# Performance work log

Measured on AMD Instinct MI355X. Metric: run time of the kernel, lower is better.

Reference implementation:

```python
import jax, jax.numpy as jnp
import numpy as np

D_MODEL = 1024
NHEAD = 16
HEAD_DIM = D_MODEL // NHEAD  # 64
Q_STRIDE = 2
KV_STRIDE = 1
ROPE_BASE = 10000.0


def _rope_tables(positions):
    # positions: [L] int -> cos/sin [L, HEAD_DIM]
    half = HEAD_DIM // 2
    inv_freq = 1.0 / (ROPE_BASE ** (jnp.arange(half, dtype=jnp.float32) / half))
    freqs = positions.astype(jnp.float32)[:, None] * inv_freq[None, :]  # [L, half]
    emb = jnp.concatenate([freqs, freqs], axis=-1)  # [L, HEAD_DIM]
    return jnp.cos(emb), jnp.sin(emb)


def _rotate_half(x):
    half = x.shape[-1] // 2
    return jnp.concatenate([-x[..., half:], x[..., :half]], axis=-1)


def _apply_rope(x, cos, sin):
    # x: [B, H, L, D]; cos/sin: [L, D] broadcast over B, H
    return x * cos + _rotate_half(x) * sin


def setup_inputs() -> dict:
    key = jax.random.key(0)
    ks = jax.random.split(key, 10)
    B, S, K = 4, 1024, 2048
    s = 0.02
    return {
        "query": jax.random.normal(ks[0], (B, S, D_MODEL), jnp.float32),
        "kv": jax.random.normal(ks[1], (B, K, D_MODEL), jnp.float32),
        "q_w": jax.random.normal(ks[2], (D_MODEL, D_MODEL), jnp.float32) * s,
        "q_b": jax.random.normal(ks[3], (D_MODEL,), jnp.float32) * s,
        "k_w": jax.random.normal(ks[4], (D_MODEL, D_MODEL), jnp.float32) * s,
        "k_b": jax.random.normal(ks[5], (D_MODEL,), jnp.float32) * s,
        "v_w": jax.random.normal(ks[6], (D_MODEL, D_MODEL), jnp.float32) * s,
        "v_b": jax.random.normal(ks[7], (D_MODEL,), jnp.float32) * s,
        "out_w": jax.random.normal(ks[8], (D_MODEL, D_MODEL), jnp.float32) * s,
        "out_b": jax.random.normal(ks[9], (D_MODEL,), jnp.float32) * s,
    }


def reference(query, kv, q_w, q_b, k_w, k_b, v_w, v_b, out_w, out_b):
    B, S, _ = query.shape
    K = kv.shape[1]
    # Projections (torch Linear: x @ W^T + b), reshape to [B, H, L, D]
    q = (query @ q_w.T + q_b).reshape(B, S, NHEAD, HEAD_DIM).transpose(0, 2, 1, 3)
    k = (kv @ k_w.T + k_b).reshape(B, K, NHEAD, HEAD_DIM).transpose(0, 2, 1, 3)
    v = (kv @ v_w.T + v_b).reshape(B, K, NHEAD, HEAD_DIM).transpose(0, 2, 1, 3)
    # RoPE at strided original frame positions
    q_cos, q_sin = _rope_tables(jnp.arange(S) * Q_STRIDE)
    k_cos, k_sin = _rope_tables(jnp.arange(K) * KV_STRIDE)
    q = _apply_rope(q, q_cos, q_sin)
    k = _apply_rope(k, k_cos, k_sin)
    scale = 1.0 / np.sqrt(HEAD_DIM).astype(np.float32)
    attn = jnp.einsum('bhsd,bhkd->bhsk', q, k) * scale  # [B, H, S, K]
    attn = jax.nn.softmax(attn, axis=-1)
    out = jnp.einsum('bhsk,bhkd->bhsd', attn, v)
    out = out.transpose(0, 2, 1, 3).reshape(B, S, D_MODEL)
    return out @ out_w.T + out_b
```

## Files before the change

kernel.cpp:

```cpp
#include <hip/hip_runtime.h>
#include <hip/hip_bf16.h>

#define D_MODEL 1024
#define NHEAD   16
#define HD      64
#define SQ      1024
#define SK      2048

typedef __attribute__((ext_vector_type(8))) short bh8;
typedef __attribute__((ext_vector_type(4))) float fx4;

#define QSCALE 0.1803368801111204f

__device__ __forceinline__ unsigned short f2bf(float f) {
  union { float f; unsigned u; } v; v.f = f;
  return (unsigned short)((v.u + 0x7FFFu + ((v.u >> 16) & 1u)) >> 16);
}

__device__ __forceinline__ float bf2f(unsigned short u) {
  union { unsigned u; float f; } v; v.u = ((unsigned)u) << 16; return v.f;
}

#define GLOAD_LDS16(gp, lp)                                                  \
  __builtin_amdgcn_global_load_lds(                                         \
      (const __attribute__((address_space(1))) unsigned int*)(gp),          \
      (__attribute__((address_space(3))) unsigned int*)(lp), 16, 0, 0)

__global__ __launch_bounds__(256) void cvt_kernel(
    const float* __restrict__ q, const float* __restrict__ kv,
    const float* __restrict__ qw, const float* __restrict__ kw,
    const float* __restrict__ vw, const float* __restrict__ ow,
    unsigned short* __restrict__ qx, unsigned short* __restrict__ kvx,
    unsigned short* __restrict__ qwx, unsigned short* __restrict__ kwx,
    unsigned short* __restrict__ vwx, unsigned short* __restrict__ owx)
{
  const int idx = blockIdx.x * 256 + threadIdx.x;
  const float* src; unsigned short* dst; size_t off;
  if (idx < 524288)        { src = q;  dst = qx;  off = idx; }
  else if (idx < 1572864)  { src = kv; dst = kvx; off = idx - 524288; }
  else {
    const int w = idx - 1572864; const int sel = w >> 17; off = w & 131071;
    src = sel == 0 ? qw : sel == 1 ? kw : sel == 2 ? vw : ow;
    dst = sel == 0 ? qwx : sel == 1 ? kwx : sel == 2 ? vwx : owx;
  }
  const float4 a = ((const float4*)src)[off * 2];
  const float4 b = ((const float4*)src)[off * 2 + 1];
  bh8 r;
  r[0] = (short)f2bf(a.x); r[1] = (short)f2bf(a.y);
  r[2] = (short)f2bf(a.z); r[3] = (short)f2bf(a.w);
  r[4] = (short)f2bf(b.x); r[5] = (short)f2bf(b.y);
  r[6] = (short)f2bf(b.z); r[7] = (short)f2bf(b.w);
  *(bh8*)(dst + off * 8) = r;
}

__global__ __launch_bounds__(256) void qkv_kernel(
    const unsigned short* __restrict__ qx, const unsigned short* __restrict__ kvx,
    const unsigned short* __restrict__ qw, const unsigned short* __restrict__ kw,
    const unsigned short* __restrict__ vw,
    const float* __restrict__ qb, const float* __restrict__ kb,
    const float* __restrict__ vb,
    unsigned short* __restrict__ outq, unsigned short* __restrict__ outk,
    unsigned short* __restrict__ outv)
{
  __shared__ unsigned short Alds[4096];
  __shared__ unsigned short Blds[8192];

  const int t = threadIdx.x;
  const int lane = t & 63, w = t >> 6;
  const int lr = lane & 15, g = lane >> 4;
  const int bid = blockIdx.x;
  const bool isQ = bid >= 2048;
  int bx, by;
  if (isQ) {
    const int tq = bid - 2048;
    const int nq = (tq & 7) * 64 + (tq >> 3);
    bx = nq & 7; by = nq >> 3;
  } else {
    const int nk = (bid & 7) * 256 + (bid >> 3);
    bx = nk & 15; by = nk >> 4;
  }
  const int row0 = by * 64;
  const int colB = bx * 128;
  const int wrow = (w >> 1) * 32;
  const int wcol = (w & 1) * 64;

  const unsigned short* X = isQ ? qx : kvx;
  const unsigned short* Wsrc; const float* bias; int colW; bool isK = false;
  if (isQ)              { Wsrc = qw; bias = qb; colW = colB; }
  else if (colB < 1024) { Wsrc = kw; bias = kb; colW = colB; isK = true; }
  else                  { Wsrc = vw; bias = vb; colW = colB - 1024; }

  const int rbase = t >> 3;
  const int sw8 = (((t & 7) ^ (rbase & 7))) * 8;
  const int sl0 = ((g) ^ (lr & 7)) * 8;
  const int sl1 = ((4 + g) ^ (lr & 7)) * 8;

  fx4 acc[2][4] = {};
  for (int k0 = 0; k0 < 1024; k0 += 64) {
    __syncthreads();
#pragma unroll
    for (int l = 0; l < 2; ++l)
      GLOAD_LDS16(X + (size_t)(row0 + rbase + l * 32) * 1024 + k0 + sw8,
                  &Alds[l * 2048 + t * 8]);
#pragma unroll
    for (int l = 0; l < 4; ++l)
      GLOAD_LDS16(Wsrc + (size_t)(colW + rbase + l * 32) * 1024 + k0 + sw8,
                  &Blds[l * 2048 + t * 8]);
    __syncthreads();

#pragma unroll
    for (int kk = 0; kk < 2; ++kk) {
      const int sl = kk ? sl1 : sl0;
      bh8 af[2], bf[4];
#pragma unroll
      for (int mi = 0; mi < 2; ++mi)
        af[mi] = *(const bh8*)&Alds[(wrow + mi * 16 + lr) * 64 + sl];
#pragma unroll
      for (int ni = 0; ni < 4; ++ni)
        bf[ni] = *(const bh8*)&Blds[(wcol + ni * 16 + lr) * 64 + sl];
      __builtin_amdgcn_s_setprio(1);
#pragma unroll
      for (int mi = 0; mi < 2; ++mi)
#pragma unroll
        for (int ni = 0; ni < 4; ++ni)
          acc[mi][ni] = __builtin_amdgcn_mfma_f32_16x16x32_bf16(af[mi], bf[ni], acc[mi][ni], 0, 0, 0);
      __builtin_amdgcn_s_setprio(0);
    }
  }

  float bv[4];
#pragma unroll
  for (int ni = 0; ni < 4; ++ni) bv[ni] = bias[colW + wcol + ni * 16 + lr];
#pragma unroll
  for (int mi = 0; mi < 2; ++mi)
#pragma unroll
    for (int ni = 0; ni < 4; ++ni)
#pragma unroll
      for (int j = 0; j < 4; ++j) acc[mi][ni][j] += bv[ni];

  const int LMASK = isQ ? 1023 : 2047;
  if (isQ || isK) {
    const float c0 = 0.41524101186092029f;
    const float invf0 = exp2f(-(float)lr * c0);
    const float invf1 = exp2f(-(float)(16 + lr) * c0);
#pragma unroll
    for (int mi = 0; mi < 2; ++mi)
#pragma unroll
      for (int j = 0; j < 4; ++j) {
        const int rg = row0 + wrow + mi * 16 + 4 * g + j;
        const int s = rg & LMASK;
        const float pos = (float)(isQ ? 2 * s : s);
#pragma unroll
        for (int ni = 0; ni < 2; ++ni) {
          float sn, cs;
          __sincosf(pos * (ni == 0 ? invf0 : invf1), &sn, &cs);
          const float x1 = acc[mi][ni][j], x2 = acc[mi][ni + 2][j];
          acc[mi][ni][j]     = x1 * cs - x2 * sn;
          acc[mi][ni + 2][j] = x2 * cs + x1 * sn;
        }
      }
  }

  const int h = (colW + wcol) >> 6;
#pragma unroll
  for (int mi = 0; mi < 2; ++mi)
#pragma unroll
    for (int j = 0; j < 4; ++j) {
      const int rg = row0 + wrow + mi * 16 + 4 * g + j;
      const int bb = isQ ? (rg >> 10) : (rg >> 11);
      const int s = rg & LMASK;
#pragma unroll
      for (int ni = 0; ni < 4; ++ni) {
        const int d = ni * 16 + lr;
        if (isQ) {
          outq[(((size_t)(bb * 16 + h)) * SQ + s) * 64 + d] = f2bf(acc[mi][ni][j] * QSCALE);
        } else {
          const size_t base = ((size_t)(bb * 16 + h)) * (SK * 64);
          if (isK)
            outk[base + (s >> 4) * 1024 + (d >> 5) * 512 + ((d >> 3) & 3) * 128 + (s & 15) * 8 + (d & 7)]
                = f2bf(acc[mi][ni][j]);
          else
            outv[base + (s >> 5) * 2048 + (d >> 4) * 512 + ((s >> 3) & 3) * 128 + (d & 15) * 8 + (s & 7)]
                = f2bf(acc[mi][ni][j]);
        }
      }
    }
}

__global__ __launch_bounds__(256) void oproj_kernel(
    const unsigned short* __restrict__ A, const unsigned short* __restrict__ W,
    const float* __restrict__ bias, float* __restrict__ out)
{
  __shared__ unsigned short Alds[4096];
  __shared__ unsigned short Blds[8192];

  const int t = threadIdx.x;
  const int lane = t & 63, w = t >> 6;
  const int lr = lane & 15, g = lane >> 4;
  const int bid = blockIdx.x;
  const int nb = (bid & 7) * 64 + (bid >> 3);
  const int bx = nb & 7, by = nb >> 3;
  const int row0 = by * 64;
  const int colB = bx * 128;
  const int wrow = (w >> 1) * 32;
  const int wcol = (w & 1) * 64;

  const int rbase = t >> 3;
  const int sw8 = (((t & 7) ^ (rbase & 7))) * 8;
  const int sl0 = ((g) ^ (lr & 7)) * 8;
  const int sl1 = ((4 + g) ^ (lr & 7)) * 8;

  fx4 acc[2][4] = {};
  for (int k0 = 0; k0 < 1024; k0 += 64) {
    __syncthreads();
#pragma unroll
    for (int l = 0; l < 2; ++l)
      GLOAD_LDS16(A + (size_t)(row0 + rbase + l * 32) * 1024 + k0 + sw8,
                  &Alds[l * 2048 + t * 8]);
#pragma unroll
    for (int l = 0; l < 4; ++l)
      GLOAD_LDS16(W + (size_t)(colB + rbase + l * 32) * 1024 + k0 + sw8,
                  &Blds[l * 2048 + t * 8]);
    __syncthreads();

#pragma unroll
    for (int kk = 0; kk < 2; ++kk) {
      const int sl = kk ? sl1 : sl0;
      bh8 af[2], bf[4];
#pragma unroll
      for (int mi = 0; mi < 2; ++mi)
        af[mi] = *(const bh8*)&Alds[(wrow + mi * 16 + lr) * 64 + sl];
#pragma unroll
      for (int ni = 0; ni < 4; ++ni)
        bf[ni] = *(const bh8*)&Blds[(wcol + ni * 16 + lr) * 64 + sl];
      __builtin_amdgcn_s_setprio(1);
#pragma unroll
      for (int mi = 0; mi < 2; ++mi)
#pragma unroll
        for (int ni = 0; ni < 4; ++ni)
          acc[mi][ni] = __builtin_amdgcn_mfma_f32_16x16x32_bf16(af[mi], bf[ni], acc[mi][ni], 0, 0, 0);
      __builtin_amdgcn_s_setprio(0);
    }
  }

  float bv[4];
#pragma unroll
  for (int ni = 0; ni < 4; ++ni) bv[ni] = bias[colB + wcol + ni * 16 + lr];
#pragma unroll
  for (int mi = 0; mi < 2; ++mi)
#pragma unroll
    for (int j = 0; j < 4; ++j) {
      const int rg = row0 + wrow + mi * 16 + 4 * g + j;
#pragma unroll
      for (int ni = 0; ni < 4; ++ni)
        out[(size_t)rg * 1024 + colB + wcol + ni * 16 + lr] = acc[mi][ni][j] + bv[ni];
    }
}

__global__ __launch_bounds__(256, 4) void attn_kernel(
    const unsigned short* __restrict__ Qr, const unsigned short* __restrict__ Kt,
    const unsigned short* __restrict__ Vt, unsigned short* __restrict__ O)
{
  __shared__ __align__(16) unsigned short smem[4 * 2304];
  __shared__ float llds[4][32];

  const int lane = threadIdx.x & 63;
  const int w = threadIdx.x >> 6;
  const int lr = lane & 15, g = lane >> 4, kl = g * 8;
  const int bid = blockIdx.x;
  const int swz = (bid & 7) * 256 + (bid >> 3);
  const int bh = swz >> 5;
  const int q0 = (swz & 31) * 32;
  const int b = bh >> 4, h = bh & 15;

  unsigned short* p_lds = smem + w * 2304;

  const unsigned short* Qp = Qr + (size_t)bh * SQ * HD;
  const unsigned short* Kp = Kt + (size_t)bh * SK * HD;
  const unsigned short* Vp = Vt + (size_t)bh * SK * HD;

  bh8 qf[2][2];
#pragma unroll
  for (int mi = 0; mi < 2; ++mi)
#pragma unroll
    for (int kk = 0; kk < 2; ++kk)
      qf[mi][kk] = *(const bh8*)(Qp + (size_t)(q0 + mi * 16 + lr) * 64 + kk * 32 + kl);

  bh8 ones;
#pragma unroll
  for (int i = 0; i < 8; ++i) ones[i] = (short)0x3F80;

  fx4 oacc[2][4] = {};
  fx4 lacc[2] = {};

  for (int t = 0; t < 8; ++t) {
    fx4 sacc[2][4] = {};
#pragma unroll
    for (int kk = 0; kk < 2; ++kk) {
      bh8 kf[4];
#pragma unroll
      for (int ni = 0; ni < 4; ++ni)
        kf[ni] = *(const bh8*)(Kp + (size_t)(w * 32 + t * 4 + ni) * 1024 + kk * 512 + g * 128 + lr * 8);
      __builtin_amdgcn_s_setprio(1);
#pragma unroll
      for (int mi = 0; mi < 2; ++mi)
#pragma unroll
        for (int ni = 0; ni < 4; ++ni)
          sacc[mi][ni] = __builtin_amdgcn_mfma_f32_16x16x32_bf16(qf[mi][kk], kf[ni], sacc[mi][ni], 0, 0, 0);
      __builtin_amdgcn_s_setprio(0);
    }

    asm volatile("s_waitcnt lgkmcnt(0)" ::: "memory");
    __builtin_amdgcn_sched_barrier(0);

#pragma unroll
    for (int mi = 0; mi < 2; ++mi)
#pragma unroll
      for (int ni = 0; ni < 4; ++ni) {
        float p0, p1, p2, p3;
        asm("v_exp_f32 %0, %1" : "=v"(p0) : "v"(sacc[mi][ni][0]));
        asm("v_exp_f32 %0, %1" : "=v"(p1) : "v"(sacc[mi][ni][1]));
        asm("v_exp_f32 %0, %1" : "=v"(p2) : "v"(sacc[mi][ni][2]));
        asm("v_exp_f32 %0, %1" : "=v"(p3) : "v"(sacc[mi][ni][3]));
        unsigned lo, hi;
        asm("v_cvt_pk_bf16_f32 %0, %1, %2" : "=v"(lo) : "v"(p0), "v"(p1));
        asm("v_cvt_pk_bf16_f32 %0, %1, %2" : "=v"(hi) : "v"(p2), "v"(p3));
        unsigned short* base = &p_lds[(mi * 16 + 4 * g) * 68 + ni * 16 + lr];
        base[0]   = (unsigned short)lo;
        base[68]  = (unsigned short)(lo >> 16);
        base[136] = (unsigned short)hi;
        base[204] = (unsigned short)(hi >> 16);
      }

    asm volatile("s_waitcnt lgkmcnt(0)" ::: "memory");
    __builtin_amdgcn_sched_barrier(0);

#pragma unroll
    for (int kk = 0; kk < 2; ++kk) {
      bh8 pa[2], vb[4];
#pragma unroll
      for (int mi = 0; mi < 2; ++mi) {
        const unsigned short* pp = &p_lds[(mi * 16 + lr) * 68 + kk * 32 + kl];
        const short4 a = *(const short4*)pp;
        const short4 c = *(const short4*)(pp + 4);
        pa[mi][0] = a.x; pa[mi][1] = a.y; pa[mi][2] = a.z; pa[mi][3] = a.w;
        pa[mi][4] = c.x; pa[mi][5] = c.y; pa[mi][6] = c.z; pa[mi][7] = c.w;
      }
#pragma unroll
      for (int ni = 0; ni < 4; ++ni)
        vb[ni] = *(const bh8*)(Vp + (size_t)(w * 16 + t * 2 + kk) * 2048 + ni * 512 + g * 128 + lr * 8);
      __builtin_amdgcn_s_setprio(1);
#pragma unroll
      for (int mi = 0; mi < 2; ++mi) {
#pragma unroll
        for (int ni = 0; ni < 4; ++ni)
          oacc[mi][ni] = __builtin_amdgcn_mfma_f32_16x16x32_bf16(pa[mi], vb[ni], oacc[mi][ni], 0, 0, 0);
        lacc[mi] = __builtin_amdgcn_mfma_f32_16x16x32_bf16(pa[mi], ones, lacc[mi], 0, 0, 0);
      }
      __builtin_amdgcn_s_setprio(0);
    }
  }

  if (lr == 0) {
#pragma unroll
    for (int mi = 0; mi < 2; ++mi)
#pragma unroll
      for (int j = 0; j < 4; ++j)
        llds[w][mi * 16 + 4 * g + j] = lacc[mi][j];
  }

  asm volatile("s_waitcnt lgkmcnt(0)" ::: "memory");
  __builtin_amdgcn_sched_barrier(0);
  unsigned short* opart = smem + w * 2304;
#pragma unroll
  for (int mi = 0; mi < 2; ++mi)
#pragma unroll
    for (int j = 0; j < 4; ++j) {
      const int row = mi * 16 + 4 * g + j;
#pragma unroll
      for (int ni = 0; ni < 4; ++ni)
        opart[row * 72 + ni * 16 + lr] = f2bf(oacc[mi][ni][j]);
    }
  __syncthreads();

  const int row = threadIdx.x >> 3;
  const int d0 = (threadIdx.x & 7) * 8;
  float a8[8] = {};
#pragma unroll
  for (int ww = 0; ww < 4; ++ww) {
    const bh8 v = *(const bh8*)(smem + ww * 2304 + row * 72 + d0);
#pragma unroll
    for (int i = 0; i < 8; ++i) a8[i] += bf2f((unsigned short)v[i]);
  }
  const float inv = 1.0f / (llds[0][row] + llds[1][row] + llds[2][row] + llds[3][row]);
  bh8 r;
#pragma unroll
  for (int i = 0; i < 8; ++i) r[i] = (short)f2bf(a8[i] * inv);
  *(bh8*)&O[((size_t)(b * SQ + q0 + row)) * D_MODEL + h * 64 + d0] = r;
}

extern "C" void kernel_launch(void* const* d_in, const int* in_sizes, int n_in,
                              void* d_out, int out_size, void* d_ws, size_t ws_size,
                              hipStream_t stream) {
  (void)in_sizes; (void)n_in; (void)out_size; (void)ws_size;
  const float* query = (const float*)d_in[0];
  const float* kv    = (const float*)d_in[1];
  const float* q_w   = (const float*)d_in[2];
  const float* q_b   = (const float*)d_in[3];
  const float* k_w   = (const float*)d_in[4];
  const float* k_b   = (const float*)d_in[5];
  const float* v_w   = (const float*)d_in[6];
  const float* v_b   = (const float*)d_in[7];
  const float* out_w = (const float*)d_in[8];
  const float* out_b = (const float*)d_in[9];
  float* out = (float*)d_out;

  unsigned short* ws = (unsigned short*)d_ws;
  unsigned short* qx     = ws;
  unsigned short* kvx    = ws + ((size_t)4  << 20);
  unsigned short* qwx    = ws + ((size_t)12 << 20);
  unsigned short* kwx    = ws + ((size_t)13 << 20);
  unsigned short* vwx    = ws + ((size_t)14 << 20);
  unsigned short* owx    = ws + ((size_t)15 << 20);
  unsigned short* q_rope = ws + ((size_t)16 << 20);
  unsigned short* k_t    = ws + ((size_t)20 << 20);
  unsigned short* v_t    = ws + ((size_t)28 << 20);
  unsigned short* attn_o = qx;

  hipLaunchKernelGGL(cvt_kernel, dim3(8192), dim3(256), 0, stream,
                     query, kv, q_w, k_w, v_w, out_w, qx, kvx, qwx, kwx, vwx, owx);
  hipLaunchKernelGGL(qkv_kernel, dim3(2560), dim3(256), 0, stream,
                     qx, kvx, qwx, kwx, vwx, q_b, k_b, v_b, q_rope, k_t, v_t);
  hipLaunchKernelGGL(attn_kernel, dim3(2048), dim3(256), 0, stream,
                     q_rope, k_t, v_t, attn_o);
  hipLaunchKernelGGL(oproj_kernel, dim3(512), dim3(256), 0, stream,
                     attn_o, owx, out_b, out);
}
```

Baseline: 143.6 us.

## Double-buffer LDS tiles in QKV and output projection GEMMs

Both projection GEMM kernels now keep two LDS buffers for the A and B tiles. Each iteration issues the asynchronous global-to-LDS loads for the next K slice before running MFMAs on the current slice, and needs one barrier per step instead of two. The aim is to hide global load latency behind matrix compute. In exchange, LDS use per block doubles to 48 KB, which may reduce how many blocks fit on each CU.

```diff
diff --git a/kernel.cpp b/kernel.cpp
--- a/kernel.cpp
+++ b/kernel.cpp
@@ -62,8 +62,8 @@
     unsigned short* __restrict__ outq, unsigned short* __restrict__ outk,
     unsigned short* __restrict__ outv)
 {
-  __shared__ unsigned short Alds[4096];
-  __shared__ unsigned short Blds[8192];
+  __shared__ unsigned short Alds[2][4096];
+  __shared__ unsigned short Blds[2][8192];
 
   const int t = threadIdx.x;
   const int lane = t & 63, w = t >> 6;
@@ -95,18 +95,23 @@
   const int sl0 = ((g) ^ (lr & 7)) * 8;
   const int sl1 = ((4 + g) ^ (lr & 7)) * 8;
 
+#define STAGE_P(k0_, bi_) do {                                                        \
+    _Pragma("unroll")                                                                 \
+    for (int l = 0; l < 2; ++l)                                                       \
+      GLOAD_LDS16(X + (size_t)(row0 + rbase + l * 32) * 1024 + (k0_) + sw8,           \
+                  &Alds[bi_][l * 2048 + t * 8]);                                      \
+    _Pragma("unroll")                                                                 \
+    for (int l = 0; l < 4; ++l)                                                       \
+      GLOAD_LDS16(Wsrc + (size_t)(colW + rbase + l * 32) * 1024 + (k0_) + sw8,        \
+                  &Blds[bi_][l * 2048 + t * 8]);                                      \
+  } while (0)
+
   fx4 acc[2][4] = {};
-  for (int k0 = 0; k0 < 1024; k0 += 64) {
+  STAGE_P(0, 0);
+  for (int kt = 0; kt < 16; ++kt) {
+    const int cur = kt & 1;
     __syncthreads();
-#pragma unroll
-    for (int l = 0; l < 2; ++l)
-      GLOAD_LDS16(X + (size_t)(row0 + rbase + l * 32) * 1024 + k0 + sw8,
-                  &Alds[l * 2048 + t * 8]);
-#pragma unroll
-    for (int l = 0; l < 4; ++l)
-      GLOAD_LDS16(Wsrc + (size_t)(colW + rbase + l * 32) * 1024 + k0 + sw8,
-                  &Blds[l * 2048 + t * 8]);
-    __syncthreads();
+    if (kt < 15) STAGE_P((kt + 1) * 64, cur ^ 1);
 
 #pragma unroll
     for (int kk = 0; kk < 2; ++kk) {
@@ -114,10 +119,10 @@
       bh8 af[2], bf[4];
 #pragma unroll
       for (int mi = 0; mi < 2; ++mi)
-        af[mi] = *(const bh8*)&Alds[(wrow + mi * 16 + lr) * 64 + sl];
-#pragma unroll
-      for (int ni = 0; ni < 4; ++ni)
-        bf[ni] = *(const bh8*)&Blds[(wcol + ni * 16 + lr) * 64 + sl];
+        af[mi] = *(const bh8*)&Alds[cur][(wrow + mi * 16 + lr) * 64 + sl];
+#pragma unroll
+      for (int ni = 0; ni < 4; ++ni)
+        bf[ni] = *(const bh8*)&Blds[cur][(wcol + ni * 16 + lr) * 64 + sl];
       __builtin_amdgcn_s_setprio(1);
 #pragma unroll
       for (int mi = 0; mi < 2; ++mi)
@@ -191,8 +196,8 @@
     const unsigned short* __restrict__ A, const unsigned short* __restrict__ W,
     const float* __restrict__ bias, float* __restrict__ out)
 {
-  __shared__ unsigned short Alds[4096];
-  __shared__ unsigned short Blds[8192];
+  __shared__ unsigned short Alds[2][4096];
+  __shared__ unsigned short Blds[2][8192];
 
   const int t = threadIdx.x;
   const int lane = t & 63, w = t >> 6;
@@ -210,18 +215,23 @@
   const int sl0 = ((g) ^ (lr & 7)) * 8;
   const int sl1 = ((4 + g) ^ (lr & 7)) * 8;
 
+#define STAGE_O(k0_, bi_) do {                                                        \
+    _Pragma("unroll")                                                                 \
+    for (int l = 0; l < 2; ++l)                                                       \
+      GLOAD_LDS16(A + (size_t)(row0 + rbase + l * 32) * 1024 + (k0_) + sw8,           \
+                  &Alds[bi_][l * 2048 + t * 8]);                                      \
+    _Pragma("unroll")                                                                 \
+    for (int l = 0; l < 4; ++l)                                                       \
+      GLOAD_LDS16(W + (size_t)(colB + rbase + l * 32) * 1024 + (k0_) + sw8,           \
+                  &Blds[bi_][l * 2048 + t * 8]);                                      \
+  } while (0)
+
   fx4 acc[2][4] = {};
-  for (int k0 = 0; k0 < 1024; k0 += 64) {
+  STAGE_O(0, 0);
+  for (int kt = 0; kt < 16; ++kt) {
+    const int cur = kt & 1;
     __syncthreads();
-#pragma unroll
-    for (int l = 0; l < 2; ++l)
-      GLOAD_LDS16(A + (size_t)(row0 + rbase + l * 32) * 1024 + k0 + sw8,
-                  &Alds[l * 2048 + t * 8]);
-#pragma unroll
-    for (int l = 0; l < 4; ++l)
-      GLOAD_LDS16(W + (size_t)(colB + rbase + l * 32) * 1024 + k0 + sw8,
-                  &Blds[l * 2048 + t * 8]);
-    __syncthreads();
+    if (kt < 15) STAGE_O((kt + 1) * 64, cur ^ 1);
 
 #pragma unroll
     for (int kk = 0; kk < 2; ++kk) {
@@ -229,10 +239,10 @@
       bh8 af[2], bf[4];
 #pragma unroll
       for (int mi = 0; mi < 2; ++mi)
-        af[mi] = *(const bh8*)&Alds[(wrow + mi * 16 + lr) * 64 + sl];
-#pragma unroll
-      for (int ni = 0; ni < 4; ++ni)
-        bf[ni] = *(const bh8*)&Blds[(wcol + ni * 16 + lr) * 64 + sl];
+        af[mi] = *(const bh8*)&Alds[cur][(wrow + mi * 16 + lr) * 64 + sl];
+#pragma unroll
+      for (int ni = 0; ni < 4; ++ni)
+        bf[ni] = *(const bh8*)&Blds[cur][(wcol + ni * 16 + lr) * 64 + sl];
       __builtin_amdgcn_s_setprio(1);
 #pragma unroll
       for (int mi = 0; mi < 2; ++mi)
```

Result: slower. 159.2 us (+10.9%).
